# Kernel optimization log

Measured on AMD Instinct MI355X. Metric: run time of the kernel, lower is better.

The kernel has to match this reference:

```python
import math
import jax, jax.numpy as jnp
import numpy as np

K = 30          # tokens per node (most recent links)
IN_CH = 100     # edge feature dim
HID = 100       # hidden channels
OUT_CH = 100    # output channels
TCH = 100       # temporal encoding dim
N = 50000       # num nodes
E = 800000      # num edges


def setup_inputs() -> dict:
    key = jax.random.key(0)
    ks = jax.random.split(key, 16)
    rn = lambda k, shape, s=0.05: (jax.random.normal(k, shape, jnp.float32) * s)
    return {
        'edge_attr': jax.random.normal(ks[0], (E, IN_CH), jnp.float32),
        'edge_time': jax.random.uniform(ks[1], (E,), jnp.float32),
        'node_batch': jax.random.randint(ks[2], (E,), 0, N, jnp.int32),
        'num_nodes': N,
        'head_w': rn(ks[3], (HID, TCH + IN_CH)), 'head_b': jnp.zeros((HID,), jnp.float32),
        'ln_t_g': jnp.ones((HID,), jnp.float32), 'ln_t_b': jnp.zeros((HID,), jnp.float32),
        'tok1_w': rn(ks[4], (K // 2, K)), 'tok1_b': jnp.zeros((K // 2,), jnp.float32),
        'tok2_w': rn(ks[5], (K, K // 2)), 'tok2_b': jnp.zeros((K,), jnp.float32),
        'ln_c_g': jnp.ones((HID,), jnp.float32), 'ln_c_b': jnp.zeros((HID,), jnp.float32),
        'ch1_w': rn(ks[6], (4 * HID, HID)), 'ch1_b': jnp.zeros((4 * HID,), jnp.float32),
        'ch2_w': rn(ks[7], (HID, 4 * HID)), 'ch2_b': jnp.zeros((HID,), jnp.float32),
        'ln_h_g': jnp.ones((HID,), jnp.float32), 'ln_h_b': jnp.zeros((HID,), jnp.float32),
        'out_w': rn(ks[8], (OUT_CH, HID)), 'out_b': jnp.zeros((OUT_CH,), jnp.float32),
    }


def _layer_norm(x, g, b, eps=1e-5):
    m = x.mean(-1, keepdims=True)
    v = ((x - m) ** 2).mean(-1, keepdims=True)
    return (x - m) * jax.lax.rsqrt(v + eps) * g + b


def _gelu(x):
    return jax.nn.gelu(x, approximate=False)  # torch default GELU is exact erf


def reference(edge_attr, edge_time, node_batch, num_nodes,
              head_w, head_b, ln_t_g, ln_t_b, tok1_w, tok1_b, tok2_w, tok2_b,
              ln_c_g, ln_c_b, ch1_w, ch1_b, ch2_w, ch2_b, ln_h_g, ln_h_b,
              out_w, out_b):
    # TemporalEncoding: cos(t * 1/sqrt(d)**linspace(0, sqrt(d), d))
    sqrt_d = math.sqrt(TCH)
    tw = 1.0 / sqrt_d ** jnp.linspace(0.0, sqrt_d, TCH)          # [TCH]
    time_info = jnp.cos(edge_time[:, None] * tw[None, :])        # [E, TCH]
    h = jnp.concatenate([time_info, edge_attr], axis=1) @ head_w.T + head_b  # [E, HID]

    # stable sort by node, take first K edges per node (PyG to_dense_batch)
    perm = jnp.argsort(node_batch)                               # stable
    nb = node_batch[perm]
    h = h[perm]
    pos = jnp.arange(nb.shape[0]) - jnp.searchsorted(nb, nb, side='left')
    idx = jnp.where(pos < K, nb * K + pos, num_nodes * K)        # overflow row -> garbage
    buf = jnp.zeros((num_nodes * K + 1, HID), h.dtype).at[idx].set(h)
    x = buf[:num_nodes * K].reshape(num_nodes, K, HID)           # [N, K, HID]

    # MLP-mixer (eval mode: dropout is identity)
    ht = _layer_norm(x, ln_t_g, ln_t_b).swapaxes(1, 2)           # [N, HID, K]
    ht = _gelu(ht @ tok1_w.T + tok1_b) @ tok2_w.T + tok2_b       # [N, HID, K]
    h_token = ht.swapaxes(1, 2) + x                              # [N, K, HID]

    hc = _layer_norm(h_token, ln_c_g, ln_c_b)
    hc = _gelu(hc @ ch1_w.T + ch1_b) @ ch2_w.T + ch2_b
    h_channel = hc + h_token                                     # [N, K, HID]

    t = _layer_norm(h_channel, ln_h_g, ln_h_b).mean(axis=1)      # [N, HID]
    return t @ out_w.T + out_b                                   # [N, OUT_CH]
```

## Files before the change

### kernel.cpp

```cpp
#include <hip/hip_runtime.h>
#include <math.h>

#define KTOK 30
#define HIDC 100
#define SB() __builtin_amdgcn_sched_barrier(0)
#define CEXP 0.33554829241286486f

typedef short s16x8 __attribute__((ext_vector_type(8)));
typedef float f32x4 __attribute__((ext_vector_type(4)));

__device__ __forceinline__ unsigned cvt_pk_bf16(float lo, float hi) {
    unsigned r;
    asm("v_cvt_pk_bf16_f32 %0, %1, %2" : "=v"(r) : "v"(lo), "v"(hi));
    return r;
}
__device__ __forceinline__ unsigned short cvt_bf16(float x) {
    unsigned r;
    asm("v_cvt_pk_bf16_f32 %0, %1, 0" : "=v"(r) : "v"(x));
    return (unsigned short)r;
}
__device__ __forceinline__ float bf2f(unsigned short h) {
    return __uint_as_float(((unsigned)h) << 16);
}
__device__ __forceinline__ float exp2_fast(float x) {
    float r;
    asm("v_exp_f32 %0, %1" : "=v"(r) : "v"(x));
    return r;
}
__device__ __forceinline__ float cos_rev(float rev) {
    float r;
    asm("v_cos_f32 %0, %1" : "=v"(r) : "v"(rev));
    return r;
}
__device__ __forceinline__ unsigned short f2bf(float f) {
    unsigned u = __float_as_uint(f);
    unsigned r = (u + 0x7FFFu + ((u >> 16) & 1u)) >> 16;
    return (unsigned short)r;
}
__device__ __forceinline__ float gelu(float x) {
    float s = x * x;
    float t = fmaf(s, 0.10294334f, 2.3022082f);
    float e = exp2_fast(-x * t);
    return x * __builtin_amdgcn_rcpf(1.0f + e);
}

__global__ void count_kernel(const int* __restrict__ nb, int* __restrict__ cnt, int E) {
    int e = blockIdx.x * blockDim.x + threadIdx.x;
    if (e < E) atomicAdd(&cnt[nb[e]], 1);
}

__global__ void scanA_kernel(const int* __restrict__ cnt, int* __restrict__ offsets,
                             int* __restrict__ bsum, int n) {
    __shared__ int sd[1024];
    int tid = threadIdx.x;
    int i = blockIdx.x * 1024 + tid;
    int v = (i < n) ? cnt[i] : 0;
    sd[tid] = v;
    __syncthreads();
    for (int off = 1; off < 1024; off <<= 1) {
        int tv = (tid >= off) ? sd[tid - off] : 0;
        __syncthreads();
        sd[tid] += tv;
        __syncthreads();
    }
    if (i < n) offsets[i] = sd[tid] - v;
    if (tid == 1023) bsum[blockIdx.x] = sd[1023];
}

__global__ void scanB_kernel(int* __restrict__ bsum, int nbk) {
    if (threadIdx.x == 0 && blockIdx.x == 0) {
        int run = 0;
        for (int b = 0; b < nbk; b++) { int tv = bsum[b]; bsum[b] = run; run += tv; }
    }
}

__global__ void scanC_kernel(int* __restrict__ offsets, const int* __restrict__ bsum, int n) {
    int i = blockIdx.x * blockDim.x + threadIdx.x;
    if (i < n) offsets[i] += bsum[i >> 10];
}

__global__ void fill_kernel(const int* __restrict__ nb, int* __restrict__ cursor,
                            const int* __restrict__ offsets, int* __restrict__ order, int E) {
    int e = blockIdx.x * blockDim.x + threadIdx.x;
    if (e >= E) return;
    int n = nb[e];
    int p = atomicAdd(&cursor[n], 1);
    order[offsets[n] + p] = e;
}

__global__ void select_kernel(const int* __restrict__ cnt, const int* __restrict__ offsets,
                              const int* __restrict__ order, int* __restrict__ sel, int N) {
    int node = blockIdx.x * blockDim.x + threadIdx.x;
    if (node >= N) return;
    int c = cnt[node];
    int off = offsets[node];
    int top[KTOK];
    int m = 0;
    for (int i = 0; i < c; i++) {
        int e = order[off + i];
        if (m < KTOK) {
            int j = m++;
            while (j > 0 && top[j - 1] > e) { top[j] = top[j - 1]; j--; }
            top[j] = e;
        } else if (e < top[KTOK - 1]) {
            int j = KTOK - 1;
            while (j > 0 && top[j - 1] > e) { top[j] = top[j - 1]; j--; }
            top[j] = e;
        }
    }
    for (int p = 0; p < KTOK; p++) sel[node * KTOK + p] = (p < m) ? top[p] : -1;
}

__global__ void prep_kernel(const float* __restrict__ head_w, const float* __restrict__ ch1_w,
                            const float* __restrict__ ch2_w, const float* __restrict__ tok1_w,
                            const float* __restrict__ tok2_w,
                            const float* __restrict__ ln_c_g, const float* __restrict__ ln_c_b,
                            const float* __restrict__ ch1_b,
                            unsigned short* __restrict__ wf,
                            float* __restrict__ Sg1, float* __restrict__ b1p) {
    int i = blockIdx.x * blockDim.x + threadIdx.x;
    if (i >= 128000) {
        int h = i - 128000;
        if (h < 400) {
            float sg = 0.f, sb = 0.f;
            for (int k = 0; k < 100; k++) {
                float w = ch1_w[h * 100 + k];
                sg += w * ln_c_g[k];
                sb += w * ln_c_b[k];
            }
            Sg1[h] = sg;
            b1p[h] = sb + ch1_b[h];
        }
        return;
    }
    float val = 0.0f;
    if (i < 28672) {
        int ii = i & 7, lane = (i >> 3) & 63, rest = i >> 9;
        int nt = rest % 7, kt = rest / 7;
        int k = kt * 32 + ((lane >> 4) << 3) + ii;
        int n = nt * 16 + (lane & 15);
        if (k < 200 && n < 100) val = head_w[n * 200 + k];
    } else if (i < 79872) {
        int j = i - 28672;
        int ii = j & 7, lane = (j >> 3) & 63, rest = j >> 9;
        int nt = rest % 25, kt = rest / 25;
        int k = kt * 32 + ((lane >> 4) << 3) + ii;
        int n = nt * 16 + (lane & 15);
        if (k < 100) val = ch1_w[n * 100 + k] * ln_c_g[k];
    } else if (i < 126464) {
        int j = i - 79872;
        int ii = j & 7, lane = (j >> 3) & 63, rest = j >> 9;
        int nt = rest % 7, kt = rest / 7;
        int k = kt * 32 + ((lane >> 4) << 3) + ii;
        int n = nt * 16 + (lane & 15);
        if (k < 400 && n < 100) val = ch2_w[n * 400 + k];
    } else if (i < 126976) {
        int j = i - 126464;
        int ii = j & 7, lane = (j >> 3) & 63;
        int k = ((lane >> 4) << 3) + ii;
        int n = lane & 15;
        if (k < 30 && n < 15) val = tok1_w[n * 30 + k];
    } else {
        int j = i - 126976;
        int ii = j & 7, lane = (j >> 3) & 63, nt = j >> 9;
        int k = ((lane >> 4) << 3) + ii;
        int n = nt * 16 + (lane & 15);
        if (k < 15 && n < 30) val = tok2_w[n * 15 + k];
    }
    wf[i] = f2bf(val);
}

__global__ __launch_bounds__(128, 3) void fused_node_kernel(
    const float* __restrict__ edge_attr, const float* __restrict__ edge_time,
    const int* __restrict__ sel, const unsigned short* __restrict__ wf,
    const float* __restrict__ head_b,
    const float* __restrict__ ln_t_g, const float* __restrict__ ln_t_b,
    const float* __restrict__ tok1_b, const float* __restrict__ tok2_b,
    const float* __restrict__ Sg1, const float* __restrict__ b1p,
    const float* __restrict__ ch2_b,
    const float* __restrict__ ln_h_g, const float* __restrict__ ln_h_b,
    const float* __restrict__ out_w, const float* __restrict__ out_b,
    float* __restrict__ out, int N) {

    __shared__ __align__(16) unsigned short xb2[2][32 * 104];
    __shared__ __align__(16) unsigned short scr2[2][1280];

    const int t = threadIdx.x;
    const int wv = t >> 6, l = t & 63;
    const int g = l >> 4, c16 = l & 15;
    unsigned short* xbw = xb2[wv];
    unsigned short* scrw = scr2[wv];
    char* scrb = (char*)scrw;
    const int node = blockIdx.x * 2 + wv;

    const s16x8 zfrag = {0, 0, 0, 0, 0, 0, 0, 0};
    const f32x4 zacc = {0.f, 0.f, 0.f, 0.f};

    const s16x8* headWf_v = (const s16x8*)(wf);
    const s16x8* wg1f_v   = (const s16x8*)(wf + 28672);
    const s16x8* w2f_v    = (const s16x8*)(wf + 79872);
    const s16x8* tok1f_v  = (const s16x8*)(wf + 126464);
    const s16x8* tok2f_v  = (const s16x8*)(wf + 126976);

    int eload = (l < KTOK && node < N) ? sel[node * KTOK + l] : -1;
    unsigned long long vmask = __ballot(eload >= 0);
    int e0 = __shfl(eload, c16);
    int e1 = __shfl(eload, 16 + c16);
    float tt0 = (e0 >= 0) ? edge_time[e0] : 0.f;
    float tt1 = (e1 >= 0) ? edge_time[e1] : 0.f;
    const float INV2PI = 0.15915494309189535f;
    float Trev0 = tt0 * INV2PI, Trev1 = tt1 * INV2PI;
    const float* ab0 = edge_attr + (size_t)(e0 < 0 ? 0 : e0) * 100;
    const float* ab1 = edge_attr + (size_t)(e1 < 0 ? 0 : e1) * 100;

    f32x4 hacc[2][7];
    #pragma unroll
    for (int a = 0; a < 2; a++)
        #pragma unroll
        for (int c = 0; c < 7; c++) hacc[a][c] = zacc;

    #pragma unroll
    for (int kc = 0; kc < 4; kc++) {
        s16x8 af[2][2];
        #pragma unroll
        for (int mt = 0; mt < 2; mt++) {
            const float Trev = mt ? Trev1 : Trev0;
            const float* abm = mt ? ab1 : ab0;
            #pragma unroll
            for (int kk = 0; kk < 2; kk++) {
                const int kb0 = kc * 64 + kk * 32;
                union { s16x8 v; unsigned u[4]; } r;
                if (kb0 + 32 <= 100) {
                    float Ab = Trev * exp2_fast(-CEXP * (float)(kb0 + g * 8));
                    #pragma unroll
                    for (int i2 = 0; i2 < 8; i2 += 2) {
                        float v0 = cos_rev(Ab * exp2f(-CEXP * (float)i2));
                        float v1 = cos_rev(Ab * exp2f(-CEXP * (float)(i2 + 1)));
                        r.u[i2 >> 1] = cvt_pk_bf16(v0, v1);
                    }
                } else if (kb0 == 96) {
                    int aoff = kb0 + g * 8 - 100;
                    int ac = aoff < 0 ? 0 : aoff;
                    const float* ap = abm + ac;
                    float4 A0 = *(const float4*)ap;
                    float4 A1 = *(const float4*)(ap + 4);
                    float fa[8] = {A0.x, A0.y, A0.z, A0.w, A1.x, A1.y, A1.z, A1.w};
                    float Ab = Trev * exp2_fast(-CEXP * (float)(kb0 + g * 8));
                    #pragma unroll
                    for (int i2 = 0; i2 < 8; i2 += 2) {
                        float cc0 = cos_rev(Ab * exp2f(-CEXP * (float)i2));
                        float cc1 = cos_rev(Ab * exp2f(-CEXP * (float)(i2 + 1)));
                        float a0 = (g == 0) ? ((i2 >= 4) ? fa[(i2 >= 4) ? i2 - 4 : 0] : 0.f) : fa[i2];
                        float a1 = (g == 0) ? ((i2 + 1 >= 4) ? fa[(i2 + 1 >= 4) ? i2 - 3 : 0] : 0.f) : fa[i2 + 1];
                        int k0 = kb0 + g * 8 + i2;
                        float v0 = (k0 < 100) ? cc0 : a0;
                        float v1 = (k0 + 1 < 100) ? cc1 : a1;
                        r.u[i2 >> 1] = cvt_pk_bf16(v0, v1);
                    }
                } else if (kb0 <= 160) {
                    int ac = kb0 + g * 8 - 100;
                    const float* ap = abm + ac;
                    float4 A0 = *(const float4*)ap;
                    float4 A1 = *(const float4*)(ap + 4);
                    r.u[0] = cvt_pk_bf16(A0.x, A0.y);
                    r.u[1] = cvt_pk_bf16(A0.z, A0.w);
                    r.u[2] = cvt_pk_bf16(A1.x, A1.y);
                    r.u[3] = cvt_pk_bf16(A1.z, A1.w);
                } else if (kb0 == 192) {
                    int aoff = kb0 + g * 8 - 100;
                    int ac = aoff > 92 ? 92 : aoff;
                    const float* ap = abm + ac;
                    float4 A0 = *(const float4*)ap;
                    float4 A1 = *(const float4*)(ap + 4);
                    float fa[8] = {A0.x, A0.y, A0.z, A0.w, A1.x, A1.y, A1.z, A1.w};
                    #pragma unroll
                    for (int i2 = 0; i2 < 8; i2 += 2) {
                        int k0 = kb0 + g * 8 + i2;
                        float v0 = (k0 < 200) ? fa[i2] : 0.f;
                        float v1 = (k0 + 1 < 200) ? fa[i2 + 1] : 0.f;
                        r.u[i2 >> 1] = cvt_pk_bf16(v0, v1);
                    }
                } else {
                    r.u[0] = 0; r.u[1] = 0; r.u[2] = 0; r.u[3] = 0;
                }
                af[mt][kk] = r.v;
            }
        }
        #pragma unroll
        for (int nt = 0; nt < 7; nt++) {
            #pragma unroll
            for (int kk = 0; kk < 2; kk++) {
                s16x8 bf = headWf_v[((kc * 2 + kk) * 7 + nt) * 64 + l];
                #pragma unroll
                for (int mt = 0; mt < 2; mt++)
                    hacc[mt][nt] = __builtin_amdgcn_mfma_f32_16x16x32_bf16(af[mt][kk], bf, hacc[mt][nt], 0, 0, 0);
            }
        }
    }

    float g7[7], b7[7], hb7[7];
    #pragma unroll
    for (int nt = 0; nt < 7; nt++) {
        int cc = nt * 16 + c16; if (cc > 99) cc = 99;
        g7[nt] = ln_t_g[cc]; b7[nt] = ln_t_b[cc]; hb7[nt] = head_b[cc];
    }

    #pragma unroll
    for (int mt = 0; mt < 2; mt++)
        #pragma unroll
        for (int nt = 0; nt < 7; nt++)
            #pragma unroll
            for (int jj = 0; jj < 4; jj++) {
                int row = mt * 16 + g * 4 + jj;
                bool ok = (((vmask >> row) & 1ull) != 0) && (nt < 6 || c16 < 4);
                hacc[mt][nt][jj] = ok ? (hacc[mt][nt][jj] + hb7[nt]) : 0.f;
            }

    #pragma unroll
    for (int mt = 0; mt < 2; mt++)
        #pragma unroll
        for (int nt = 0; nt < 7; nt++)
            #pragma unroll
            for (int jj = 0; jj < 4; jj++) {
                int row = mt * 16 + g * 4 + jj;
                int col = nt * 16 + c16;
                if (col < 100)      xbw[row * 104 + col] = cvt_bf16(hacc[mt][nt][jj]);
                else if (col < 104) xbw[row * 104 + col] = 0;
            }

    float mv[2][4], rv[2][4];
    #pragma unroll
    for (int mt = 0; mt < 2; mt++)
        #pragma unroll
        for (int jj = 0; jj < 4; jj++) {
            float s = 0.f, s2 = 0.f;
            #pragma unroll
            for (int nt = 0; nt < 7; nt++) {
                float v = hacc[mt][nt][jj];
                s += v;
                s2 = fmaf(v, v, s2);
            }
            #pragma unroll
            for (int msk = 1; msk < 16; msk <<= 1) {
                s  += __shfl_xor(s, msk);
                s2 += __shfl_xor(s2, msk);
            }
            float m = s * 0.01f;
            float var = fmaxf(s2 * 0.01f - m * m, 0.f);
            mv[mt][jj] = m;
            rv[mt][jj] = rsqrtf(var + 1e-5f);
        }

    s16x8 av[7];
    #pragma unroll
    for (int nb = 0; nb < 4; nb++) {
        #pragma unroll
        for (int nn = 0; nn < 2; nn++) {
            int nt = nb * 2 + nn;
            if (nt < 7) {
                #pragma unroll
                for (int mt = 0; mt < 2; mt++) {
                    float h0 = fmaf((hacc[mt][nt][0] - mv[mt][0]) * rv[mt][0], g7[nt], b7[nt]);
                    float h1 = fmaf((hacc[mt][nt][1] - mv[mt][1]) * rv[mt][1], g7[nt], b7[nt]);
                    float h2 = fmaf((hacc[mt][nt][2] - mv[mt][2]) * rv[mt][2], g7[nt], b7[nt]);
                    float h3 = fmaf((hacc[mt][nt][3] - mv[mt][3]) * rv[mt][3], g7[nt], b7[nt]);
                    unsigned w0 = cvt_pk_bf16(h0, h1);
                    unsigned w1 = cvt_pk_bf16(h2, h3);
                    int ba = (nt & 1) * 1024 + (c16 + 32 * mt + 16 * (g >> 1)) * 16 + 8 * (g & 1);
                    *(uint2*)(scrb + ba) = make_uint2(w0, w1);
                }
            }
        }
        SB();
        #pragma unroll
        for (int nn = 0; nn < 2; nn++) {
            int nt = nb * 2 + nn;
            if (nt < 7)
                av[nt] = *(const s16x8*)(scrb + (nt & 1) * 1024 + l * 16);
        }
        SB();
    }

    {
        s16x8 b1 = tok1f_v[l];
        float bias1 = (c16 < 15) ? tok1_b[c16] : 0.f;
        s16x8 b2a = tok2f_v[l];
        s16x8 b2b = tok2f_v[64 + l];
        float tb0 = tok2_b[c16];
        float tb1 = (c16 < 14) ? tok2_b[16 + c16] : 0.f;
        #pragma unroll
        for (int mt7 = 0; mt7 < 7; mt7++) {
            f32x4 y = __builtin_amdgcn_mfma_f32_16x16x32_bf16(av[mt7], b1, zacc, 0, 0, 0);
            #pragma unroll
            for (int jj = 0; jj < 4; jj++) {
                int ba = ((g * 4 + jj) + (c16 >> 3) * 16) * 16 + (c16 & 7) * 2;
                *(unsigned short*)(scrb + ba) = cvt_bf16(gelu(y[jj] + bias1));
            }
            SB();
            s16x8 a2 = zfrag;
            if (g < 2) a2 = *(const s16x8*)(scrb + l * 16);
            SB();
            f32x4 d0 = __builtin_amdgcn_mfma_f32_16x16x32_bf16(a2, b2a, zacc, 0, 0, 0);
            f32x4 d1 = __builtin_amdgcn_mfma_f32_16x16x32_bf16(a2, b2b, zacc, 0, 0, 0);
            #pragma unroll
            for (int jj = 0; jj < 4; jj++) {
                int chD = mt7 * 16 + g * 4 + jj;
                if (chD < 100) {
                    int idx0 = c16 * 104 + chD;
                    xbw[idx0] = cvt_bf16(bf2f(xbw[idx0]) + d0[jj] + tb0);
                    int tok1i = 16 + c16;
                    if (tok1i < 30) {
                        int idx1 = tok1i * 104 + chD;
                        xbw[idx1] = cvt_bf16(bf2f(xbw[idx1]) + d1[jj] + tb1);
                    }
                }
            }
            SB();
        }
    }

    unsigned short* cbw = scrw;
    f32x4 acc2[2][7];
    {
        s16x8 a1f[2][4];
        #pragma unroll
        for (int mt = 0; mt < 2; mt++)
            #pragma unroll
            for (int kk = 0; kk < 4; kk++) {
                s16x8 a = zfrag;
                if (kk < 3 || g == 0)
                    a = *(const s16x8*)&xbw[(mt * 16 + c16) * 104 + kk * 32 + g * 8];
                a1f[mt][kk] = a;
            }
        SB();

        float rs_r[2][4], rm_r[2][4];
        {
            float mA[2], rA[2];
            #pragma unroll
            for (int mt = 0; mt < 2; mt++) {
                float s = 0.f, s2 = 0.f;
                #pragma unroll
                for (int kk = 0; kk < 4; kk++)
                    #pragma unroll
                    for (int i = 0; i < 8; i++) {
                        float f = bf2f((unsigned short)a1f[mt][kk][i]);
                        s += f;
                        s2 = fmaf(f, f, s2);
                    }
                s  += __shfl_xor(s, 16);  s  += __shfl_xor(s, 32);
                s2 += __shfl_xor(s2, 16); s2 += __shfl_xor(s2, 32);
                float m = s * 0.01f;
                float var = fmaxf(s2 * 0.01f - m * m, 0.f);
                mA[mt] = m;
                rA[mt] = rsqrtf(var + 1e-5f);
            }
            #pragma unroll
            for (int mt = 0; mt < 2; mt++)
                #pragma unroll
                for (int jj = 0; jj < 4; jj++) {
                    int src = g * 4 + jj;
                    float mm = __shfl(mA[mt], src);
                    float rr = __shfl(rA[mt], src);
                    rs_r[mt][jj] = rr;
                    rm_r[mt][jj] = rr * mm;
                }
        }

        #pragma unroll
        for (int a = 0; a < 2; a++)
            #pragma unroll
            for (int c = 0; c < 7; c++) acc2[a][c] = zacc;

        for (int hc = 0; hc < 13; hc++) {
            f32x4 acc1[2][2];
            float Sg[2], Bp[2];
            #pragma unroll
            for (int a = 0; a < 2; a++) { acc1[a][0] = zacc; acc1[a][1] = zacc; }
            #pragma unroll
            for (int ntl = 0; ntl < 2; ntl++) {
                int ntg = hc * 2 + ntl;
                if (ntg < 25) {
                    int h = ntg * 16 + c16;
                    Sg[ntl] = Sg1[h];
                    Bp[ntl] = b1p[h];
                    #pragma unroll
                    for (int kk = 0; kk < 4; kk++) {
                        s16x8 bfr = wg1f_v[(kk * 25 + ntg) * 64 + l];
                        #pragma unroll
                        for (int mt = 0; mt < 2; mt++)
                            acc1[mt][ntl] = __builtin_amdgcn_mfma_f32_16x16x32_bf16(a1f[mt][kk], bfr, acc1[mt][ntl], 0, 0, 0);
                    }
                }
            }
            #pragma unroll
            for (int ntl = 0; ntl < 2; ntl++) {
                int ntg = hc * 2 + ntl;
                if (ntg < 25) {
                    #pragma unroll
                    for (int mt = 0; mt < 2; mt++)
                        #pragma unroll
                        for (int jj = 0; jj < 4; jj++) {
                            int row = mt * 16 + g * 4 + jj;
                            float h1 = fmaf(rs_r[mt][jj], acc1[mt][ntl][jj],
                                            fmaf(-rm_r[mt][jj], Sg[ntl], Bp[ntl]));
                            cbw[row * 40 + ntl * 16 + c16] = cvt_bf16(gelu(h1));
                        }
                }
            }
            SB();
            s16x8 a2f[2];
            #pragma unroll
            for (int mt = 0; mt < 2; mt++)
                a2f[mt] = *(const s16x8*)&cbw[(mt * 16 + c16) * 40 + g * 8];
            SB();
            #pragma unroll
            for (int nt2 = 0; nt2 < 7; nt2++) {
                s16x8 b2f = w2f_v[(hc * 7 + nt2) * 64 + l];
                #pragma unroll
                for (int mt = 0; mt < 2; mt++)
                    acc2[mt][nt2] = __builtin_amdgcn_mfma_f32_16x16x32_bf16(a2f[mt], b2f, acc2[mt][nt2], 0, 0, 0);
            }
            SB();
        }
    }

    #pragma unroll
    for (int nt = 0; nt < 7; nt++) {
        int col = nt * 16 + c16;
        if (col < 100) {
            float bias = ch2_b[col];
            #pragma unroll
            for (int mt = 0; mt < 2; mt++)
                #pragma unroll
                for (int jj = 0; jj < 4; jj++) {
                    int row = mt * 16 + g * 4 + jj;
                    acc2[mt][nt][jj] += bias + bf2f(xbw[row * 104 + col]);
                }
        }
    }
    float m_[2][4], rs_[2][4];
    #pragma unroll
    for (int mt = 0; mt < 2; mt++)
        #pragma unroll
        for (int jj = 0; jj < 4; jj++) {
            float s = 0.f, s2 = 0.f;
            #pragma unroll
            for (int nt = 0; nt < 7; nt++) {
                float v = acc2[mt][nt][jj];
                s += v;
                s2 = fmaf(v, v, s2);
            }
            #pragma unroll
            for (int msk = 1; msk < 16; msk <<= 1) {
                s  += __shfl_xor(s, msk);
                s2 += __shfl_xor(s2, msk);
            }
            float m = s * 0.01f;
            float var = fmaxf(s2 * 0.01f - m * m, 0.f);
            m_[mt][jj]  = m;
            rs_[mt][jj] = rsqrtf(var + 1e-5f);
        }
    float cs[7];
    #pragma unroll
    for (int nt = 0; nt < 7; nt++) cs[nt] = 0.f;
    #pragma unroll
    for (int mt = 0; mt < 2; mt++)
        #pragma unroll
        for (int jj = 0; jj < 4; jj++) {
            int row = mt * 16 + g * 4 + jj;
            if (row < 30) {
                float m = m_[mt][jj], rs = rs_[mt][jj];
                #pragma unroll
                for (int nt = 0; nt < 7; nt++)
                    cs[nt] = fmaf(acc2[mt][nt][jj] - m, rs, cs[nt]);
            }
        }
    #pragma unroll
    for (int nt = 0; nt < 7; nt++) {
        cs[nt] += __shfl_xor(cs[nt], 16);
        cs[nt] += __shfl_xor(cs[nt], 32);
    }
    float* stF = (float*)scrw;
    if (g == 0) {
        #pragma unroll
        for (int nt = 0; nt < 7; nt++) {
            int col = nt * 16 + c16;
            if (col < 100)
                stF[col] = ln_h_g[col] * cs[nt] * (1.0f / 30.0f) + ln_h_b[col];
        }
    }
    SB();
    #pragma unroll
    for (int p = 0; p < 2; p++) {
        int o = p * 64 + l;
        if (o < 100 && node < N) {
            float a = out_b[o];
            const float* wr = out_w + o * 100;
            #pragma unroll
            for (int c = 0; c < 100; c += 4) {
                float4 w4 = *(const float4*)(wr + c);
                f32x4 t4 = *(const f32x4*)&stF[c];
                a += w4.x * t4[0] + w4.y * t4[1] + w4.z * t4[2] + w4.w * t4[3];
            }
            out[(size_t)node * 100 + o] = a;
        }
    }
}


extern "C" void kernel_launch(void* const* d_in, const int* in_sizes, int n_in,
                              void* d_out, int out_size, void* d_ws, size_t ws_size,
                              hipStream_t stream) {
    const float* edge_attr  = (const float*)d_in[0];
    const float* edge_time  = (const float*)d_in[1];
    const int*   node_batch = (const int*)d_in[2];
    const float* head_w = (const float*)d_in[4];
    const float* head_b = (const float*)d_in[5];
    const float* ln_t_g = (const float*)d_in[6];
    const float* ln_t_b = (const float*)d_in[7];
    const float* tok1_w = (const float*)d_in[8];
    const float* tok1_b = (const float*)d_in[9];
    const float* tok2_w = (const float*)d_in[10];
    const float* tok2_b = (const float*)d_in[11];
    const float* ln_c_g = (const float*)d_in[12];
    const float* ln_c_b = (const float*)d_in[13];
    const float* ch1_w  = (const float*)d_in[14];
    const float* ch1_b  = (const float*)d_in[15];
    const float* ch2_w  = (const float*)d_in[16];
    const float* ch2_b  = (const float*)d_in[17];
    const float* ln_h_g = (const float*)d_in[18];
    const float* ln_h_b = (const float*)d_in[19];
    const float* out_w  = (const float*)d_in[20];
    const float* out_b  = (const float*)d_in[21];
    float* out = (float*)d_out;

    const int E = in_sizes[2];
    const int N = out_size / HIDC;

    int* cnt     = (int*)d_ws;
    int* cursor  = cnt + N;
    int* offsets = cursor + N;
    int* order   = offsets + N;
    int* sel     = order + E;
    unsigned short* wf = (unsigned short*)(sel + (size_t)N * KTOK);
    float* Sg1 = (float*)(wf + 128000);
    float* b1p = Sg1 + 400;
    int*   bsum = (int*)(b1p + 400);

    const int nbk = (N + 1023) / 1024;

    hipMemsetAsync(cnt, 0, (size_t)2 * N * sizeof(int), stream);
    count_kernel<<<(E + 255) / 256, 256, 0, stream>>>(node_batch, cnt, E);
    scanA_kernel<<<nbk, 1024, 0, stream>>>(cnt, offsets, bsum, N);
    scanB_kernel<<<1, 64, 0, stream>>>(bsum, nbk);
    scanC_kernel<<<(N + 255) / 256, 256, 0, stream>>>(offsets, bsum, N);
    fill_kernel<<<(E + 255) / 256, 256, 0, stream>>>(node_batch, cursor, offsets, order, E);
    select_kernel<<<(N + 255) / 256, 256, 0, stream>>>(cnt, offsets, order, sel, N);
    prep_kernel<<<502, 256, 0, stream>>>(head_w, ch1_w, ch2_w, tok1_w, tok2_w,
                                         ln_c_g, ln_c_b, ch1_b, wf, Sg1, b1p);
    fused_node_kernel<<<(N + 1) / 2, 128, 0, stream>>>(
        edge_attr, edge_time, sel, wf, head_b,
        ln_t_g, ln_t_b, tok1_b, tok2_b, Sg1, b1p,
        ch2_b, ln_h_g, ln_h_b, out_w, out_b, out, N);
}
```

Baseline: 1.132 ms.

## Double-buffer channel-MLP scratch, batch token-mixer stages, skip zero K-chunk in head GEMM

Doubles the per-wave LDS scratch so the channel MLP writes GELU output of chunk hc into one buffer while the second GEMM consumes chunk hc-1 from the other, software-pipelining the two matmuls and removing a barrier per iteration. The token-mixer first stage now computes all seven tiles into scratch before the second stage reads them, instead of alternating per tile with sched barriers. The LN-to-transpose staging is regrouped into 4+3 tiles to cut barrier rounds. The head GEMM skips the all-zero last K sub-chunk. Larger LDS use per block may lower occupancy.

New measurement: 1.064 ms. -6.0%, faster.

```diff
diff --git a/kernel.cpp b/kernel.cpp
--- a/kernel.cpp
+++ b/kernel.cpp
@@ -183,7 +183,7 @@
     float* __restrict__ out, int N) {
 
     __shared__ __align__(16) unsigned short xb2[2][32 * 104];
-    __shared__ __align__(16) unsigned short scr2[2][1280];
+    __shared__ __align__(16) unsigned short scr2[2][2560];
 
     const int t = threadIdx.x;
     const int wv = t >> 6, l = t & 63;
@@ -229,6 +229,7 @@
             #pragma unroll
             for (int kk = 0; kk < 2; kk++) {
                 const int kb0 = kc * 64 + kk * 32;
+                if (kb0 >= 224) { af[mt][kk] = zfrag; continue; }
                 union { s16x8 v; unsigned u[4]; } r;
                 if (kb0 + 32 <= 100) {
                     float Ab = Trev * exp2_fast(-CEXP * (float)(kb0 + g * 8));
@@ -266,7 +267,7 @@
                     r.u[1] = cvt_pk_bf16(A0.z, A0.w);
                     r.u[2] = cvt_pk_bf16(A1.x, A1.y);
                     r.u[3] = cvt_pk_bf16(A1.z, A1.w);
-                } else if (kb0 == 192) {
+                } else {
                     int aoff = kb0 + g * 8 - 100;
                     int ac = aoff > 92 ? 92 : aoff;
                     const float* ap = abm + ac;
@@ -280,8 +281,6 @@
                         float v1 = (k0 + 1 < 200) ? fa[i2 + 1] : 0.f;
                         r.u[i2 >> 1] = cvt_pk_bf16(v0, v1);
                     }
-                } else {
-                    r.u[0] = 0; r.u[1] = 0; r.u[2] = 0; r.u[3] = 0;
                 }
                 af[mt][kk] = r.v;
             }
@@ -290,6 +289,7 @@
         for (int nt = 0; nt < 7; nt++) {
             #pragma unroll
             for (int kk = 0; kk < 2; kk++) {
+                if (kc == 3 && kk == 1) continue;
                 s16x8 bf = headWf_v[((kc * 2 + kk) * 7 + nt) * 64 + l];
                 #pragma unroll
                 for (int mt = 0; mt < 2; mt++)
@@ -353,11 +353,13 @@
 
     s16x8 av[7];
     #pragma unroll
-    for (int nb = 0; nb < 4; nb++) {
-        #pragma unroll
-        for (int nn = 0; nn < 2; nn++) {
-            int nt = nb * 2 + nn;
-            if (nt < 7) {
+    for (int nb = 0; nb < 2; nb++) {
+        const int nt0 = nb ? 4 : 0;
+        const int ntN = nb ? 3 : 4;
+        #pragma unroll
+        for (int nn = 0; nn < 4; nn++) {
+            if (nn < ntN) {
+                int nt = nt0 + nn;
                 #pragma unroll
                 for (int mt = 0; mt < 2; mt++) {
                     float h0 = fmaf((hacc[mt][nt][0] - mv[mt][0]) * rv[mt][0], g7[nt], b7[nt]);
@@ -366,17 +368,16 @@
                     float h3 = fmaf((hacc[mt][nt][3] - mv[mt][3]) * rv[mt][3], g7[nt], b7[nt]);
                     unsigned w0 = cvt_pk_bf16(h0, h1);
                     unsigned w1 = cvt_pk_bf16(h2, h3);
-                    int ba = (nt & 1) * 1024 + (c16 + 32 * mt + 16 * (g >> 1)) * 16 + 8 * (g & 1);
+                    int ba = nn * 1024 + (c16 + 32 * mt + 16 * (g >> 1)) * 16 + 8 * (g & 1);
                     *(uint2*)(scrb + ba) = make_uint2(w0, w1);
                 }
             }
         }
         SB();
         #pragma unroll
-        for (int nn = 0; nn < 2; nn++) {
-            int nt = nb * 2 + nn;
-            if (nt < 7)
-                av[nt] = *(const s16x8*)(scrb + (nt & 1) * 1024 + l * 16);
+        for (int nn = 0; nn < 4; nn++) {
+            if (nn < ntN)
+                av[nt0 + nn] = *(const s16x8*)(scrb + nn * 1024 + l * 16);
         }
         SB();
     }
@@ -384,22 +385,24 @@
     {
         s16x8 b1 = tok1f_v[l];
         float bias1 = (c16 < 15) ? tok1_b[c16] : 0.f;
+        #pragma unroll
+        for (int mt7 = 0; mt7 < 7; mt7++) {
+            f32x4 y = __builtin_amdgcn_mfma_f32_16x16x32_bf16(av[mt7], b1, zacc, 0, 0, 0);
+            #pragma unroll
+            for (int jj = 0; jj < 4; jj++) {
+                int ba = mt7 * 512 + (((g * 4 + jj) + (c16 >> 3) * 16) * 16 + (c16 & 7) * 2);
+                *(unsigned short*)(scrb + ba) = cvt_bf16(gelu(y[jj] + bias1));
+            }
+        }
+        SB();
         s16x8 b2a = tok2f_v[l];
         s16x8 b2b = tok2f_v[64 + l];
         float tb0 = tok2_b[c16];
         float tb1 = (c16 < 14) ? tok2_b[16 + c16] : 0.f;
         #pragma unroll
         for (int mt7 = 0; mt7 < 7; mt7++) {
-            f32x4 y = __builtin_amdgcn_mfma_f32_16x16x32_bf16(av[mt7], b1, zacc, 0, 0, 0);
-            #pragma unroll
-            for (int jj = 0; jj < 4; jj++) {
-                int ba = ((g * 4 + jj) + (c16 >> 3) * 16) * 16 + (c16 & 7) * 2;
-                *(unsigned short*)(scrb + ba) = cvt_bf16(gelu(y[jj] + bias1));
-            }
-            SB();
             s16x8 a2 = zfrag;
-            if (g < 2) a2 = *(const s16x8*)(scrb + l * 16);
-            SB();
+            if (g < 2) a2 = *(const s16x8*)(scrb + mt7 * 512 + l * 16);
             f32x4 d0 = __builtin_amdgcn_mfma_f32_16x16x32_bf16(a2, b2a, zacc, 0, 0, 0);
             f32x4 d1 = __builtin_amdgcn_mfma_f32_16x16x32_bf16(a2, b2b, zacc, 0, 0, 0);
             #pragma unroll
@@ -415,11 +418,12 @@
                     }
                 }
             }
-            SB();
-        }
-    }
-
-    unsigned short* cbw = scrw;
+        }
+        SB();
+    }
+
+    unsigned short* cbw0 = scrw;
+    unsigned short* cbw1 = scrw + 1280;
     f32x4 acc2[2][7];
     {
         s16x8 a1f[2][4];
@@ -473,6 +477,7 @@
             for (int c = 0; c < 7; c++) acc2[a][c] = zacc;
 
         for (int hc = 0; hc < 13; hc++) {
+            unsigned short* cw = (hc & 1) ? cbw1 : cbw0;
             f32x4 acc1[2][2];
             float Sg[2], Bp[2];
             #pragma unroll
@@ -504,19 +509,35 @@
                             int row = mt * 16 + g * 4 + jj;
                             float h1 = fmaf(rs_r[mt][jj], acc1[mt][ntl][jj],
                                             fmaf(-rm_r[mt][jj], Sg[ntl], Bp[ntl]));
-                            cbw[row * 40 + ntl * 16 + c16] = cvt_bf16(gelu(h1));
+                            cw[row * 40 + ntl * 16 + c16] = cvt_bf16(gelu(h1));
                         }
                 }
             }
             SB();
+            if (hc > 0) {
+                unsigned short* cr = (hc & 1) ? cbw0 : cbw1;
+                s16x8 a2f[2];
+                #pragma unroll
+                for (int mt = 0; mt < 2; mt++)
+                    a2f[mt] = *(const s16x8*)&cr[(mt * 16 + c16) * 40 + g * 8];
+                #pragma unroll
+                for (int nt2 = 0; nt2 < 7; nt2++) {
+                    s16x8 b2f = w2f_v[((hc - 1) * 7 + nt2) * 64 + l];
+                    #pragma unroll
+                    for (int mt = 0; mt < 2; mt++)
+                        acc2[mt][nt2] = __builtin_amdgcn_mfma_f32_16x16x32_bf16(a2f[mt], b2f, acc2[mt][nt2], 0, 0, 0);
+                }
+            }
+            SB();
+        }
+        {
             s16x8 a2f[2];
             #pragma unroll
             for (int mt = 0; mt < 2; mt++)
-                a2f[mt] = *(const s16x8*)&cbw[(mt * 16 + c16) * 40 + g * 8];
-            SB();
+                a2f[mt] = *(const s16x8*)&cbw0[(mt * 16 + c16) * 40 + g * 8];
             #pragma unroll
             for (int nt2 = 0; nt2 < 7; nt2++) {
-                s16x8 b2f = w2f_v[(hc * 7 + nt2) * 64 + l];
+                s16x8 b2f = w2f_v[(12 * 7 + nt2) * 64 + l];
                 #pragma unroll
                 for (int mt = 0; mt < 2; mt++)
                     acc2[mt][nt2] = __builtin_amdgcn_mfma_f32_16x16x32_bf16(a2f[mt], b2f, acc2[mt][nt2], 0, 0, 0);
```
